# Optimization experiments

Measured on AMD Instinct MI355X. Metric: run time of the kernel, lower is better.

The kernel has to match this reference:

```python
import jax, jax.numpy as jnp
import numpy as np

EPS = 1e-7
ALPHA, GAMMA = 1.0, 2.0
W_CLASS, W_BBOX, W_GIOU, W_CUT = 1.0, 5.0, 2.0, 3.0
FN_PENALTY = 10.0
N = 4194304


def setup_inputs() -> dict:
    key = jax.random.key(0)
    k = jax.random.split(key, 6)
    return {
        "pred_logits": jax.random.normal(k[0], (N, 4), dtype=jnp.float32),
        "target_labels": jax.random.randint(k[1], (N,), 0, 4, dtype=jnp.int64),
        "pred_boxes": jax.random.uniform(k[2], (N, 4), dtype=jnp.float32),
        "target_boxes": jax.random.uniform(k[3], (N, 4), dtype=jnp.float32),
        "cutting_logits": jax.random.normal(k[4], (N,), dtype=jnp.float32),
        "cutting_targets": (jax.random.uniform(k[5], (N,)) < 0.3).astype(jnp.float32),
    }


def _focal_loss(logits, labels):
    # F.cross_entropy per-sample, then focal reweighting
    logp = jax.nn.log_softmax(logits, axis=-1)
    ce = -jnp.take_along_axis(logp, labels[:, None], axis=-1)[:, 0]
    pt = jnp.exp(-ce)
    return jnp.mean(ALPHA * (1.0 - pt) ** GAMMA * ce)


def _validate_and_fix(boxes):
    # _validate_and_fix_boxes: clamp(min=0) for rows with x1>x2 or y1>y2
    invalid = (boxes[:, 0] > boxes[:, 2]) | (boxes[:, 1] > boxes[:, 3])
    boxes = jnp.where(invalid[:, None], jnp.maximum(boxes, 0.0), boxes)
    # _fix_invalid_boxes inside generalized_box_iou: x2>=x1+1e-6, y2>=y1+1e-6
    x1, y1, x2, y2 = boxes[:, 0], boxes[:, 1], boxes[:, 2], boxes[:, 3]
    x2 = jnp.maximum(x2, x1 + 1e-6)
    y2 = jnp.maximum(y2, y1 + 1e-6)
    return jnp.stack([x1, y1, x2, y2], axis=1)


def _giou_loss(pred_boxes, target_boxes):
    # Matched-pair GIoU: same math as diag(generalized_box_iou(p, t)),
    # computed elementwise instead of materializing the [N,N] matrix.
    b1 = _validate_and_fix(pred_boxes)
    b2 = _validate_and_fix(target_boxes)
    area1 = (b1[:, 2] - b1[:, 0]) * (b1[:, 3] - b1[:, 1])
    area2 = (b2[:, 2] - b2[:, 0]) * (b2[:, 3] - b2[:, 1])
    lt = jnp.maximum(b1[:, :2], b2[:, :2])
    rb = jnp.minimum(b1[:, 2:], b2[:, 2:])
    wh = jnp.maximum(rb - lt, 0.0)
    inter = wh[:, 0] * wh[:, 1]
    union = area1 + area2 - inter
    iou = inter / (union + EPS)
    lt_e = jnp.minimum(b1[:, :2], b2[:, :2])
    rb_e = jnp.maximum(b1[:, 2:], b2[:, 2:])
    wh_e = jnp.maximum(rb_e - lt_e, 0.0)
    enclosing = wh_e[:, 0] * wh_e[:, 1]
    giou = iou - (enclosing - union) / (enclosing + EPS)
    return jnp.mean(jnp.maximum(1.0 - giou, 0.0))


def _weighted_bce(logits, targets):
    # BCEWithLogits, stable form
    bce = jnp.maximum(logits, 0.0) - logits * targets + jnp.log1p(jnp.exp(-jnp.abs(logits)))
    probs = jax.nn.sigmoid(logits)
    fn_mask = (targets == 1.0) & (probs < 0.5)
    weights = jnp.where(fn_mask, FN_PENALTY, 1.0)
    return jnp.mean(bce * weights)


def reference(pred_logits, target_labels, pred_boxes, target_boxes, cutting_logits, cutting_targets):
    loss_class = jnp.maximum(_focal_loss(pred_logits, target_labels), 0.0)
    loss_bbox = jnp.maximum(jnp.mean(jnp.abs(pred_boxes - target_boxes)), 0.0)
    loss_giou = jnp.maximum(_giou_loss(pred_boxes, target_boxes), 0.0)
    loss_cutting = jnp.maximum(_weighted_bce(cutting_logits, cutting_targets), 0.0)
    total = (W_CLASS * loss_class + W_BBOX * loss_bbox
             + W_GIOU * loss_giou + W_CUT * loss_cutting)
    return total, loss_class, loss_bbox, loss_giou, loss_cutting
```

## Files before the change

### kernel.cpp

```cpp
#include <hip/hip_runtime.h>
#include <math.h>

#define EPS 1e-7f
#define FN_PENALTY 10.0f
#define BLOCK 256

__device__ __forceinline__ float waveReduceSum(float v) {
    #pragma unroll
    for (int off = 32; off > 0; off >>= 1)
        v += __shfl_down(v, off, 64);
    return v;
}

__device__ __forceinline__ float4 validate_fix(float4 b) {
    bool invalid = (b.x > b.z) || (b.y > b.w);
    if (invalid) {
        b.x = fmaxf(b.x, 0.0f);
        b.y = fmaxf(b.y, 0.0f);
        b.z = fmaxf(b.z, 0.0f);
        b.w = fmaxf(b.w, 0.0f);
    }
    b.z = fmaxf(b.z, b.x + 1e-6f);
    b.w = fmaxf(b.w, b.y + 1e-6f);
    return b;
}

__device__ __forceinline__ void accum_row(
    float4 lg, int lbl, float4 pb, float4 tb, float cl, float ct,
    float& s_class, float& s_bbox, float& s_giou, float& s_cut)
{
    float l0 = lg.x, l1 = lg.y, l2 = lg.z, l3 = lg.w;
    float m = fmaxf(fmaxf(l0, l1), fmaxf(l2, l3));
    float se = __expf(l0 - m) + __expf(l1 - m) + __expf(l2 - m) + __expf(l3 - m);
    float lse = m + __logf(se);
    lbl &= 3;
    float lsel = (lbl == 0) ? l0 : (lbl == 1) ? l1 : (lbl == 2) ? l2 : l3;
    float ce = lse - lsel;
    float pt = __expf(-ce);
    float om = 1.0f - pt;
    s_class += om * om * ce;

    s_bbox += fabsf(pb.x - tb.x) + fabsf(pb.y - tb.y)
            + fabsf(pb.z - tb.z) + fabsf(pb.w - tb.w);

    float4 b1 = validate_fix(pb);
    float4 b2 = validate_fix(tb);
    float area1 = (b1.z - b1.x) * (b1.w - b1.y);
    float area2 = (b2.z - b2.x) * (b2.w - b2.y);
    float ltx = fmaxf(b1.x, b2.x), lty = fmaxf(b1.y, b2.y);
    float rbx = fminf(b1.z, b2.z), rby = fminf(b1.w, b2.w);
    float iw = fmaxf(rbx - ltx, 0.0f), ih = fmaxf(rby - lty, 0.0f);
    float inter = iw * ih;
    float uni = area1 + area2 - inter;
    float iou = inter / (uni + EPS);
    float ex1 = fminf(b1.x, b2.x), ey1 = fminf(b1.y, b2.y);
    float ex2 = fmaxf(b1.z, b2.z), ey2 = fmaxf(b1.w, b2.w);
    float ew = fmaxf(ex2 - ex1, 0.0f), eh = fmaxf(ey2 - ey1, 0.0f);
    float enc = ew * eh;
    float giou = iou - (enc - uni) / (enc + EPS);
    s_giou += fmaxf(1.0f - giou, 0.0f);

    float bce = fmaxf(cl, 0.0f) - cl * ct + __logf(1.0f + __expf(-fabsf(cl)));
    float w = ((ct == 1.0f) && (cl < 0.0f)) ? FN_PENALTY : 1.0f;
    s_cut += bce * w;
}

__device__ __forceinline__ void block_reduce_store(
    float s_class, float s_bbox, float s_giou, float s_cut,
    float4* __restrict__ out_slot)
{
    s_class = waveReduceSum(s_class);
    s_bbox  = waveReduceSum(s_bbox);
    s_giou  = waveReduceSum(s_giou);
    s_cut   = waveReduceSum(s_cut);

    __shared__ float red[4][4];
    const int lane = threadIdx.x & 63;
    const int wave = threadIdx.x >> 6;
    if (lane == 0) {
        red[wave][0] = s_class;
        red[wave][1] = s_bbox;
        red[wave][2] = s_giou;
        red[wave][3] = s_cut;
    }
    __syncthreads();
    if (threadIdx.x == 0) {
        float4 r;
        r.x = red[0][0] + red[1][0] + red[2][0] + red[3][0];
        r.y = red[0][1] + red[1][1] + red[2][1] + red[3][1];
        r.z = red[0][2] + red[1][2] + red[2][2] + red[3][2];
        r.w = red[0][3] + red[1][3] + red[2][3] + red[3][3];
        *out_slot = r;
    }
}

__global__ __launch_bounds__(BLOCK) void loss_reduce(
    const float4* __restrict__ pred_logits,
    const int*    __restrict__ labels,
    const float4* __restrict__ pred_boxes,
    const float4* __restrict__ target_boxes,
    const float*  __restrict__ cut_logits,
    const float*  __restrict__ cut_targets,
    float4* __restrict__ block_out, int n)
{
    const int i = blockIdx.x * BLOCK + threadIdx.x;
    float s_class = 0.0f, s_bbox = 0.0f, s_giou = 0.0f, s_cut = 0.0f;
    if (i < n) {
        accum_row(pred_logits[i], labels[i], pred_boxes[i], target_boxes[i],
                  cut_logits[i], cut_targets[i],
                  s_class, s_bbox, s_giou, s_cut);
    }
    block_reduce_store(s_class, s_bbox, s_giou, s_cut, &block_out[blockIdx.x]);
}

__global__ __launch_bounds__(BLOCK) void reduce_partials(
    const float4* __restrict__ in, int n, float4* __restrict__ out)
{
    float c = 0.0f, b = 0.0f, g = 0.0f, u = 0.0f;
    for (int i = blockIdx.x * BLOCK + threadIdx.x; i < n; i += gridDim.x * BLOCK) {
        float4 r = in[i];
        c += r.x; b += r.y; g += r.z; u += r.w;
    }
    block_reduce_store(c, b, g, u, &out[blockIdx.x]);
}

__global__ void finalize_kernel(const float4* __restrict__ in, int n,
                                float* __restrict__ out, float inv_n)
{
    const int lane = threadIdx.x & 63;
    float c = 0.0f, b = 0.0f, g = 0.0f, u = 0.0f;
    for (int i = lane; i < n; i += 64) {
        float4 r = in[i];
        c += r.x; b += r.y; g += r.z; u += r.w;
    }
    c = waveReduceSum(c);
    b = waveReduceSum(b);
    g = waveReduceSum(g);
    u = waveReduceSum(u);
    if (lane == 0) {
        float lc   = fmaxf(c * inv_n, 0.0f);
        float lb   = fmaxf(b * inv_n * 0.25f, 0.0f);
        float lg   = fmaxf(g * inv_n, 0.0f);
        float lcut = fmaxf(u * inv_n, 0.0f);
        float total = 1.0f * lc + 5.0f * lb + 2.0f * lg + 3.0f * lcut;
        out[0] = total;
        out[1] = lc;
        out[2] = lb;
        out[3] = lg;
        out[4] = lcut;
    }
}

extern "C" void kernel_launch(void* const* d_in, const int* in_sizes, int n_in,
                              void* d_out, int out_size, void* d_ws, size_t ws_size,
                              hipStream_t stream) {
    const float4* pred_logits  = (const float4*)d_in[0];
    const int*    labels       = (const int*)d_in[1];
    const float4* pred_boxes   = (const float4*)d_in[2];
    const float4* target_boxes = (const float4*)d_in[3];
    const float*  cut_logits   = (const float*)d_in[4];
    const float*  cut_targets  = (const float*)d_in[5];
    float4* ws4 = (float4*)d_ws;
    float*  out = (float*)d_out;
    const int n = in_sizes[1];

    const int grid1 = (n + BLOCK - 1) / BLOCK;
    const int grid2 = 64;
    float4* part1 = ws4;
    float4* part2 = ws4 + grid1;

    loss_reduce<<<grid1, BLOCK, 0, stream>>>(pred_logits, labels, pred_boxes,
                                             target_boxes, cut_logits, cut_targets,
                                             part1, n);
    reduce_partials<<<grid2, BLOCK, 0, stream>>>(part1, grid1, part2);
    finalize_kernel<<<1, 64, 0, stream>>>(part2, grid2, out, 1.0f / (float)n);
}
```

Baseline: 234.0 us.

## Use grid-stride loop with software-prefetched rows and cheaper focal/GIoU math

Replaces the one-row-per-thread launch with a fixed 2048-block grid-stride loop that loads the next row before computing the current one, so memory latency overlaps with arithmetic. It also computes pt directly from the softmax exponentials, avoiding one exp, and switches the divisions to fast __fdividef. Launch bounds now request 8 blocks per CU. Register pressure from the double-buffered row may limit occupancy, and the fast divides are slightly less accurate.

```diff
diff --git a/kernel.cpp b/kernel.cpp
--- a/kernel.cpp
+++ b/kernel.cpp
@@ -25,26 +25,52 @@
     return b;
 }
 
+struct Row {
+    float4 lg, pb, tb;
+    float  cl, ct;
+    int    lbl;
+};
+
+__device__ __forceinline__ Row load_row(
+    const float4* __restrict__ pred_logits,
+    const int*    __restrict__ labels,
+    const float4* __restrict__ pred_boxes,
+    const float4* __restrict__ target_boxes,
+    const float*  __restrict__ cut_logits,
+    const float*  __restrict__ cut_targets,
+    int i)
+{
+    Row r;
+    r.lg  = pred_logits[i];
+    r.lbl = labels[i];
+    r.pb  = pred_boxes[i];
+    r.tb  = target_boxes[i];
+    r.cl  = cut_logits[i];
+    r.ct  = cut_targets[i];
+    return r;
+}
+
 __device__ __forceinline__ void accum_row(
-    float4 lg, int lbl, float4 pb, float4 tb, float cl, float ct,
+    const Row& r,
     float& s_class, float& s_bbox, float& s_giou, float& s_cut)
 {
-    float l0 = lg.x, l1 = lg.y, l2 = lg.z, l3 = lg.w;
+    float l0 = r.lg.x, l1 = r.lg.y, l2 = r.lg.z, l3 = r.lg.w;
     float m = fmaxf(fmaxf(l0, l1), fmaxf(l2, l3));
-    float se = __expf(l0 - m) + __expf(l1 - m) + __expf(l2 - m) + __expf(l3 - m);
-    float lse = m + __logf(se);
-    lbl &= 3;
-    float lsel = (lbl == 0) ? l0 : (lbl == 1) ? l1 : (lbl == 2) ? l2 : l3;
-    float ce = lse - lsel;
-    float pt = __expf(-ce);
+    float e0 = __expf(l0 - m), e1 = __expf(l1 - m),
+          e2 = __expf(l2 - m), e3 = __expf(l3 - m);
+    float se = e0 + e1 + e2 + e3;
+    int lbl = r.lbl & 3;
+    float esel = (lbl == 0) ? e0 : (lbl == 1) ? e1 : (lbl == 2) ? e2 : e3;
+    float pt = __fdividef(esel, se);
+    float ce = -__logf(pt);
     float om = 1.0f - pt;
     s_class += om * om * ce;
 
-    s_bbox += fabsf(pb.x - tb.x) + fabsf(pb.y - tb.y)
-            + fabsf(pb.z - tb.z) + fabsf(pb.w - tb.w);
-
-    float4 b1 = validate_fix(pb);
-    float4 b2 = validate_fix(tb);
+    s_bbox += fabsf(r.pb.x - r.tb.x) + fabsf(r.pb.y - r.tb.y)
+            + fabsf(r.pb.z - r.tb.z) + fabsf(r.pb.w - r.tb.w);
+
+    float4 b1 = validate_fix(r.pb);
+    float4 b2 = validate_fix(r.tb);
     float area1 = (b1.z - b1.x) * (b1.w - b1.y);
     float area2 = (b2.z - b2.x) * (b2.w - b2.y);
     float ltx = fmaxf(b1.x, b2.x), lty = fmaxf(b1.y, b2.y);
@@ -52,14 +78,15 @@
     float iw = fmaxf(rbx - ltx, 0.0f), ih = fmaxf(rby - lty, 0.0f);
     float inter = iw * ih;
     float uni = area1 + area2 - inter;
-    float iou = inter / (uni + EPS);
+    float iou = __fdividef(inter, uni + EPS);
     float ex1 = fminf(b1.x, b2.x), ey1 = fminf(b1.y, b2.y);
     float ex2 = fmaxf(b1.z, b2.z), ey2 = fmaxf(b1.w, b2.w);
     float ew = fmaxf(ex2 - ex1, 0.0f), eh = fmaxf(ey2 - ey1, 0.0f);
     float enc = ew * eh;
-    float giou = iou - (enc - uni) / (enc + EPS);
+    float giou = iou - __fdividef(enc - uni, enc + EPS);
     s_giou += fmaxf(1.0f - giou, 0.0f);
 
+    float cl = r.cl, ct = r.ct;
     float bce = fmaxf(cl, 0.0f) - cl * ct + __logf(1.0f + __expf(-fabsf(cl)));
     float w = ((ct == 1.0f) && (cl < 0.0f)) ? FN_PENALTY : 1.0f;
     s_cut += bce * w;
@@ -94,7 +121,7 @@
     }
 }
 
-__global__ __launch_bounds__(BLOCK) void loss_reduce(
+__global__ __launch_bounds__(BLOCK, 8) void loss_reduce(
     const float4* __restrict__ pred_logits,
     const int*    __restrict__ labels,
     const float4* __restrict__ pred_boxes,
@@ -103,13 +130,24 @@
     const float*  __restrict__ cut_targets,
     float4* __restrict__ block_out, int n)
 {
-    const int i = blockIdx.x * BLOCK + threadIdx.x;
     float s_class = 0.0f, s_bbox = 0.0f, s_giou = 0.0f, s_cut = 0.0f;
+    const int stride = gridDim.x * BLOCK;
+    int i = blockIdx.x * BLOCK + threadIdx.x;
+
     if (i < n) {
-        accum_row(pred_logits[i], labels[i], pred_boxes[i], target_boxes[i],
-                  cut_logits[i], cut_targets[i],
-                  s_class, s_bbox, s_giou, s_cut);
-    }
+        Row cur = load_row(pred_logits, labels, pred_boxes, target_boxes,
+                           cut_logits, cut_targets, i);
+        int nx = i + stride;
+        while (nx < n) {
+            Row nxt = load_row(pred_logits, labels, pred_boxes, target_boxes,
+                               cut_logits, cut_targets, nx);
+            accum_row(cur, s_class, s_bbox, s_giou, s_cut);
+            cur = nxt;
+            nx += stride;
+        }
+        accum_row(cur, s_class, s_bbox, s_giou, s_cut);
+    }
+
     block_reduce_store(s_class, s_bbox, s_giou, s_cut, &block_out[blockIdx.x]);
 }
 
@@ -164,7 +202,7 @@
     float*  out = (float*)d_out;
     const int n = in_sizes[1];
 
-    const int grid1 = (n + BLOCK - 1) / BLOCK;
+    const int grid1 = 2048;
     const int grid2 = 64;
     float4* part1 = ws4;
     float4* part2 = ws4 + grid1;
```

New measurement: 238.0 us. No clear change (+1.7%).

## Split loss reduction into specialized block groups per loss with grid-stride loops

Applied to the files above, without the earlier changes.

Replaces the one-row-per-thread kernel with a fixed grid of 4096 blocks split into three groups. Each group runs a grid-stride loop over one loss: box L1+GIoU, focal, or the cutting BCE, which uses float4 vector loads. Group sizes follow each loss's bytes read, aiming to balance memory traffic and shrink the partial-sum array and launch count. It also swaps GIoU divisions for __fdividef, giving up a little precision.

```diff
diff --git a/kernel.cpp b/kernel.cpp
--- a/kernel.cpp
+++ b/kernel.cpp
@@ -4,6 +4,11 @@
 #define EPS 1e-7f
 #define FN_PENALTY 10.0f
 #define BLOCK 256
+
+#define GRID1    4096
+#define NB_BOX   2176
+#define NB_FOCAL 1376
+#define NB_CUT   544
 
 __device__ __forceinline__ float waveReduceSum(float v) {
     #pragma unroll
@@ -25,44 +30,10 @@
     return b;
 }
 
-__device__ __forceinline__ void accum_row(
-    float4 lg, int lbl, float4 pb, float4 tb, float cl, float ct,
-    float& s_class, float& s_bbox, float& s_giou, float& s_cut)
-{
-    float l0 = lg.x, l1 = lg.y, l2 = lg.z, l3 = lg.w;
-    float m = fmaxf(fmaxf(l0, l1), fmaxf(l2, l3));
-    float se = __expf(l0 - m) + __expf(l1 - m) + __expf(l2 - m) + __expf(l3 - m);
-    float lse = m + __logf(se);
-    lbl &= 3;
-    float lsel = (lbl == 0) ? l0 : (lbl == 1) ? l1 : (lbl == 2) ? l2 : l3;
-    float ce = lse - lsel;
-    float pt = __expf(-ce);
-    float om = 1.0f - pt;
-    s_class += om * om * ce;
-
-    s_bbox += fabsf(pb.x - tb.x) + fabsf(pb.y - tb.y)
-            + fabsf(pb.z - tb.z) + fabsf(pb.w - tb.w);
-
-    float4 b1 = validate_fix(pb);
-    float4 b2 = validate_fix(tb);
-    float area1 = (b1.z - b1.x) * (b1.w - b1.y);
-    float area2 = (b2.z - b2.x) * (b2.w - b2.y);
-    float ltx = fmaxf(b1.x, b2.x), lty = fmaxf(b1.y, b2.y);
-    float rbx = fminf(b1.z, b2.z), rby = fminf(b1.w, b2.w);
-    float iw = fmaxf(rbx - ltx, 0.0f), ih = fmaxf(rby - lty, 0.0f);
-    float inter = iw * ih;
-    float uni = area1 + area2 - inter;
-    float iou = inter / (uni + EPS);
-    float ex1 = fminf(b1.x, b2.x), ey1 = fminf(b1.y, b2.y);
-    float ex2 = fmaxf(b1.z, b2.z), ey2 = fmaxf(b1.w, b2.w);
-    float ew = fmaxf(ex2 - ex1, 0.0f), eh = fmaxf(ey2 - ey1, 0.0f);
-    float enc = ew * eh;
-    float giou = iou - (enc - uni) / (enc + EPS);
-    s_giou += fmaxf(1.0f - giou, 0.0f);
-
+__device__ __forceinline__ float bce_term(float cl, float ct) {
     float bce = fmaxf(cl, 0.0f) - cl * ct + __logf(1.0f + __expf(-fabsf(cl)));
     float w = ((ct == 1.0f) && (cl < 0.0f)) ? FN_PENALTY : 1.0f;
-    s_cut += bce * w;
+    return bce * w;
 }
 
 __device__ __forceinline__ void block_reduce_store(
@@ -103,13 +74,69 @@
     const float*  __restrict__ cut_targets,
     float4* __restrict__ block_out, int n)
 {
-    const int i = blockIdx.x * BLOCK + threadIdx.x;
+    const int b = blockIdx.x;
     float s_class = 0.0f, s_bbox = 0.0f, s_giou = 0.0f, s_cut = 0.0f;
-    if (i < n) {
-        accum_row(pred_logits[i], labels[i], pred_boxes[i], target_boxes[i],
-                  cut_logits[i], cut_targets[i],
-                  s_class, s_bbox, s_giou, s_cut);
-    }
+
+    if (b < NB_BOX) {
+        const int stride = NB_BOX * BLOCK;
+        for (int i = b * BLOCK + threadIdx.x; i < n; i += stride) {
+            float4 pb = pred_boxes[i];
+            float4 tb = target_boxes[i];
+
+            s_bbox += fabsf(pb.x - tb.x) + fabsf(pb.y - tb.y)
+                    + fabsf(pb.z - tb.z) + fabsf(pb.w - tb.w);
+
+            float4 b1 = validate_fix(pb);
+            float4 b2 = validate_fix(tb);
+            float area1 = (b1.z - b1.x) * (b1.w - b1.y);
+            float area2 = (b2.z - b2.x) * (b2.w - b2.y);
+            float ltx = fmaxf(b1.x, b2.x), lty = fmaxf(b1.y, b2.y);
+            float rbx = fminf(b1.z, b2.z), rby = fminf(b1.w, b2.w);
+            float iw = fmaxf(rbx - ltx, 0.0f), ih = fmaxf(rby - lty, 0.0f);
+            float inter = iw * ih;
+            float uni = area1 + area2 - inter;
+            float iou = __fdividef(inter, uni + EPS);
+            float ex1 = fminf(b1.x, b2.x), ey1 = fminf(b1.y, b2.y);
+            float ex2 = fmaxf(b1.z, b2.z), ey2 = fmaxf(b1.w, b2.w);
+            float ew = fmaxf(ex2 - ex1, 0.0f), eh = fmaxf(ey2 - ey1, 0.0f);
+            float enc = ew * eh;
+            float giou = iou - __fdividef(enc - uni, enc + EPS);
+            s_giou += fmaxf(1.0f - giou, 0.0f);
+        }
+    } else if (b < NB_BOX + NB_FOCAL) {
+        const int stride = NB_FOCAL * BLOCK;
+        for (int i = (b - NB_BOX) * BLOCK + threadIdx.x; i < n; i += stride) {
+            float4 lg = pred_logits[i];
+            int lbl = labels[i] & 3;
+            float l0 = lg.x, l1 = lg.y, l2 = lg.z, l3 = lg.w;
+            float m = fmaxf(fmaxf(l0, l1), fmaxf(l2, l3));
+            float e0 = __expf(l0 - m), e1 = __expf(l1 - m),
+                  e2 = __expf(l2 - m), e3 = __expf(l3 - m);
+            float se = e0 + e1 + e2 + e3;
+            float lsel = (lbl == 0) ? l0 : (lbl == 1) ? l1 : (lbl == 2) ? l2 : l3;
+            float ce = __logf(se) + m - lsel;
+            float pt = __expf(-ce);
+            float om = 1.0f - pt;
+            s_class += om * om * ce;
+        }
+    } else {
+        const int stride = NB_CUT * BLOCK;
+        const int n4 = n >> 2;
+        const float4* cl4 = (const float4*)cut_logits;
+        const float4* ct4 = (const float4*)cut_targets;
+        int t = (b - NB_BOX - NB_FOCAL) * BLOCK + threadIdx.x;
+        for (int i = t; i < n4; i += stride) {
+            float4 a = cl4[i];
+            float4 c = ct4[i];
+            s_cut += bce_term(a.x, c.x) + bce_term(a.y, c.y)
+                   + bce_term(a.z, c.z) + bce_term(a.w, c.w);
+        }
+        if (t == 0) {
+            for (int i = n4 << 2; i < n; ++i)
+                s_cut += bce_term(cut_logits[i], cut_targets[i]);
+        }
+    }
+
     block_reduce_store(s_class, s_bbox, s_giou, s_cut, &block_out[blockIdx.x]);
 }
 
@@ -164,14 +191,13 @@
     float*  out = (float*)d_out;
     const int n = in_sizes[1];
 
-    const int grid1 = (n + BLOCK - 1) / BLOCK;
     const int grid2 = 64;
     float4* part1 = ws4;
-    float4* part2 = ws4 + grid1;
-
-    loss_reduce<<<grid1, BLOCK, 0, stream>>>(pred_logits, labels, pred_boxes,
+    float4* part2 = ws4 + GRID1;
+
+    loss_reduce<<<GRID1, BLOCK, 0, stream>>>(pred_logits, labels, pred_boxes,
                                              target_boxes, cut_logits, cut_targets,
                                              part1, n);
-    reduce_partials<<<grid2, BLOCK, 0, stream>>>(part1, grid1, part2);
+    reduce_partials<<<grid2, BLOCK, 0, stream>>>(part1, GRID1, part2);
     finalize_kernel<<<1, 64, 0, stream>>>(part2, grid2, out, 1.0f / (float)n);
 }
```

After: 236.3 us. About the same (+1.0%).

## Use grid-stride loop with 2x unrolled nontemporal loads and fixed grid

Applied to the files above, without the earlier changes.

Replaces one-row-per-thread launch with a fixed 2048-block grid-stride loop that processes two rows per iteration, issuing all loads up front as nontemporal loads to increase memory-level parallelism and avoid cache pollution. Also swaps IEEE divisions for __fdividef and slightly reorders the log-sum-exp. Fewer partials cut the second-stage reduction work, at the cost of possibly lower occupancy-driven latency hiding and small accuracy changes from fast division.

```diff
diff --git a/kernel.cpp b/kernel.cpp
--- a/kernel.cpp
+++ b/kernel.cpp
@@ -4,6 +4,21 @@
 #define EPS 1e-7f
 #define FN_PENALTY 10.0f
 #define BLOCK 256
+
+typedef float  vf4 __attribute__((ext_vector_type(4)));
+typedef int    vi4 __attribute__((ext_vector_type(4)));
+
+__device__ __forceinline__ float4 ntload4f(const float4* p) {
+    vf4 v = __builtin_nontemporal_load((const vf4*)p);
+    float4 r; r.x = v.x; r.y = v.y; r.z = v.z; r.w = v.w;
+    return r;
+}
+__device__ __forceinline__ int ntloadi(const int* p) {
+    return __builtin_nontemporal_load(p);
+}
+__device__ __forceinline__ float ntloadf(const float* p) {
+    return __builtin_nontemporal_load(p);
+}
 
 __device__ __forceinline__ float waveReduceSum(float v) {
     #pragma unroll
@@ -31,11 +46,12 @@
 {
     float l0 = lg.x, l1 = lg.y, l2 = lg.z, l3 = lg.w;
     float m = fmaxf(fmaxf(l0, l1), fmaxf(l2, l3));
-    float se = __expf(l0 - m) + __expf(l1 - m) + __expf(l2 - m) + __expf(l3 - m);
-    float lse = m + __logf(se);
+    float e0 = __expf(l0 - m), e1 = __expf(l1 - m),
+          e2 = __expf(l2 - m), e3 = __expf(l3 - m);
+    float se = e0 + e1 + e2 + e3;
     lbl &= 3;
     float lsel = (lbl == 0) ? l0 : (lbl == 1) ? l1 : (lbl == 2) ? l2 : l3;
-    float ce = lse - lsel;
+    float ce = __logf(se) + m - lsel;
     float pt = __expf(-ce);
     float om = 1.0f - pt;
     s_class += om * om * ce;
@@ -52,12 +68,12 @@
     float iw = fmaxf(rbx - ltx, 0.0f), ih = fmaxf(rby - lty, 0.0f);
     float inter = iw * ih;
     float uni = area1 + area2 - inter;
-    float iou = inter / (uni + EPS);
+    float iou = __fdividef(inter, uni + EPS);
     float ex1 = fminf(b1.x, b2.x), ey1 = fminf(b1.y, b2.y);
     float ex2 = fmaxf(b1.z, b2.z), ey2 = fmaxf(b1.w, b2.w);
     float ew = fmaxf(ex2 - ex1, 0.0f), eh = fmaxf(ey2 - ey1, 0.0f);
     float enc = ew * eh;
-    float giou = iou - (enc - uni) / (enc + EPS);
+    float giou = iou - __fdividef(enc - uni, enc + EPS);
     s_giou += fmaxf(1.0f - giou, 0.0f);
 
     float bce = fmaxf(cl, 0.0f) - cl * ct + __logf(1.0f + __expf(-fabsf(cl)));
@@ -103,13 +119,36 @@
     const float*  __restrict__ cut_targets,
     float4* __restrict__ block_out, int n)
 {
-    const int i = blockIdx.x * BLOCK + threadIdx.x;
     float s_class = 0.0f, s_bbox = 0.0f, s_giou = 0.0f, s_cut = 0.0f;
+    const int stride  = gridDim.x * BLOCK;
+    const int stride2 = stride * 2;
+    int i = blockIdx.x * BLOCK + threadIdx.x;
+
+    for (; i + stride < n; i += stride2) {
+        const int j = i + stride;
+        float4 lgA = ntload4f(&pred_logits[i]);
+        float4 lgB = ntload4f(&pred_logits[j]);
+        float4 pbA = ntload4f(&pred_boxes[i]);
+        float4 pbB = ntload4f(&pred_boxes[j]);
+        float4 tbA = ntload4f(&target_boxes[i]);
+        float4 tbB = ntload4f(&target_boxes[j]);
+        int    lbA = ntloadi(&labels[i]);
+        int    lbB = ntloadi(&labels[j]);
+        float  clA = ntloadf(&cut_logits[i]);
+        float  clB = ntloadf(&cut_logits[j]);
+        float  ctA = ntloadf(&cut_targets[i]);
+        float  ctB = ntloadf(&cut_targets[j]);
+
+        accum_row(lgA, lbA, pbA, tbA, clA, ctA, s_class, s_bbox, s_giou, s_cut);
+        accum_row(lgB, lbB, pbB, tbB, clB, ctB, s_class, s_bbox, s_giou, s_cut);
+    }
     if (i < n) {
-        accum_row(pred_logits[i], labels[i], pred_boxes[i], target_boxes[i],
-                  cut_logits[i], cut_targets[i],
+        accum_row(ntload4f(&pred_logits[i]), ntloadi(&labels[i]),
+                  ntload4f(&pred_boxes[i]), ntload4f(&target_boxes[i]),
+                  ntloadf(&cut_logits[i]), ntloadf(&cut_targets[i]),
                   s_class, s_bbox, s_giou, s_cut);
     }
+
     block_reduce_store(s_class, s_bbox, s_giou, s_cut, &block_out[blockIdx.x]);
 }
 
@@ -164,7 +203,7 @@
     float*  out = (float*)d_out;
     const int n = in_sizes[1];
 
-    const int grid1 = (n + BLOCK - 1) / BLOCK;
+    const int grid1 = 2048;
     const int grid2 = 64;
     float4* part1 = ws4;
     float4* part2 = ws4 + grid1;
```

Result: faster. 217.6 us (-7.0%).
